# Optimization experiments

Hardware: AMD Instinct MI355X
Metric: run time of the kernel (lower is better)

## Reference

```python
import jax, jax.numpy as jnp
import numpy as np

D = 300       # word_embedding_dim
H = 15        # num_attention_heads
DK = D // H   # 20 per-head dim
QDIM = 200    # query_vector_dim (additive attention)
N_ITEMS = 100000
B, S = 1024, 50


def setup_inputs() -> dict:
    key = jax.random.key(0)
    ks = jax.random.split(key, 16)
    sc = 1.0 / np.sqrt(D)
    inp = {
        "user_news_id": jax.random.randint(ks[0], (B, S), 0, N_ITEMS, dtype=jnp.int64 if jax.config.jax_enable_x64 else jnp.int32),
        "user_vector": jax.random.normal(ks[1], (B, S, D), dtype=jnp.float32),
        # news-id embedding table, padding_idx=0 -> zero row
        "emb_table": jax.random.normal(ks[2], (N_ITEMS + 1, D), dtype=jnp.float32).at[0].set(0.0) * 0.02,
        # content Q/K/V projections
        "Wq": jax.random.normal(ks[3], (D, D), dtype=jnp.float32) * sc,
        "bq": jnp.zeros((D,), jnp.float32),
        "Wk": jax.random.normal(ks[4], (D, D), dtype=jnp.float32) * sc,
        "bk": jnp.zeros((D,), jnp.float32),
        "Wv": jax.random.normal(ks[5], (D, D), dtype=jnp.float32) * sc,
        "bv": jnp.zeros((D,), jnp.float32),
        # disentangled (news-id) Q/K projections
        "Wqp": jax.random.normal(ks[6], (D, D), dtype=jnp.float32) * sc,
        "bqp": jnp.zeros((D,), jnp.float32),
        "Wkp": jax.random.normal(ks[7], (D, D), dtype=jnp.float32) * sc,
        "bkp": jnp.zeros((D,), jnp.float32),
        # additive attention pooling params
        "W_add": jax.random.normal(ks[8], (D, QDIM), dtype=jnp.float32) * sc,
        "b_add": jnp.zeros((QDIM,), jnp.float32),
        "q_add": jax.random.normal(ks[9], (QDIM,), dtype=jnp.float32) * (1.0 / np.sqrt(QDIM)),
    }
    return inp


def _heads(x):
    # [B,S,D] -> [B,H,S,DK]
    b, s, _ = x.shape
    return x.reshape(b, s, H, DK).transpose(0, 2, 1, 3)


def reference(user_news_id, user_vector, emb_table, Wq, bq, Wk, bk, Wv, bv,
              Wqp, bqp, Wkp, bkp, W_add, b_add, q_add):
    # embedding lookup for clicked-news ids
    user_emb = emb_table[user_news_id]                      # [B,S,D]

    # content projections from user_vector, position/id projections from user_emb
    Qc = _heads(user_vector @ Wq + bq)
    Kc = _heads(user_vector @ Wk + bk)
    Vc = _heads(user_vector @ Wv + bv)
    Qp = _heads(user_emb @ Wqp + bqp)
    Kp = _heads(user_emb @ Wkp + bkp)

    # disentangled scores: content->content + content->id + id->content
    scores = (jnp.einsum("bhqd,bhkd->bhqk", Qc, Kc)
              + jnp.einsum("bhqd,bhkd->bhqk", Qc, Kp)
              + jnp.einsum("bhqd,bhkd->bhqk", Qp, Kc))
    scores = scores * (1.0 / np.sqrt(3.0 * DK))
    attn = jax.nn.softmax(scores, axis=-1)                  # [B,H,S,S]
    ctx = jnp.einsum("bhqk,bhkd->bhqd", attn, Vc)           # [B,H,S,DK]
    ctx = ctx.transpose(0, 2, 1, 3).reshape(user_vector.shape)  # [B,S,D]

    # additive attention pooling over the sequence
    t = jnp.tanh(ctx @ W_add + b_add)                       # [B,S,QDIM]
    a = jax.nn.softmax(t @ q_add, axis=-1)                  # [B,S]
    return jnp.einsum("bs,bsd->bd", a, ctx)                 # [B,D]
```

## Files before the change

### kernel.cpp

```cpp
#include <hip/hip_runtime.h>
#include <hip/hip_bf16.h>

#define SS   50
#define DD   300
#define NH   15
#define HD   20
#define QDIM 200

#define WSEG  97280
#define WAOFF 486400
#define WTOT  552960

typedef __attribute__((ext_vector_type(8)))  short bf8t;
typedef __attribute__((ext_vector_type(4)))  float f4t;
typedef __attribute__((ext_vector_type(16))) float f16t;

__device__ __forceinline__ unsigned short f2bf(float x){
  unsigned u = __float_as_uint(x);
  return (unsigned short)((u + 0x7fffu + ((u >> 16) & 1u)) >> 16);
}
__device__ __forceinline__ unsigned packbf(float a, float b){
  return (unsigned)f2bf(a) | ((unsigned)f2bf(b) << 16);
}
__device__ __forceinline__ f16t zero16(){
  f16t v;
  #pragma unroll
  for (int i = 0; i < 16; ++i) v[i] = 0.f;
  return v;
}

__global__ __launch_bounds__(256) void conv_weights(
    const float* __restrict__ Wq, const float* __restrict__ Wk,
    const float* __restrict__ Wv, const float* __restrict__ Wqp,
    const float* __restrict__ Wkp, const float* __restrict__ Wa,
    short* __restrict__ ws)
{
  int idx = blockIdx.x*256 + threadIdx.x;
  if (idx >= WTOT) return;
  float v = 0.f;
  if (idx < WAOFF){
    int seg = idx / WSEG, r = idx - seg*WSEG;
    int n = r / 320, k = r - n*320;
    const float* W = (seg==0)?Wq:(seg==1)?Wk:(seg==2)?Wv:(seg==3)?Wqp:Wkp;
    if (n < DD && k < DD) v = W[k*DD + n];
  } else {
    int r = idx - WAOFF;
    int n = r / 320, k = r - n*320;
    if (n < QDIM && k < DD) v = Wa[k*QDIM + n];
  }
  ws[idx] = (short)f2bf(v);
}

template<int NT, int NCTM>
__device__ __forceinline__ void gemm10(const unsigned char* sm, unsigned abase,
                                       const short* __restrict__ wt,
                                       int lane, int w, f4t (&acc)[NT][4])
{
  const int lm = lane & 15, lg = lane >> 4;
  #pragma unroll
  for (int step = 0; step < 10; ++step){
    bf8t a[4];
    #pragma unroll
    for (int rt = 0; rt < 4; ++rt)
      a[rt] = *(const bf8t*)(sm + abase + (unsigned)(rt*16 + lm)*656u + (unsigned)(step*32 + lg*8)*2u);
    #pragma unroll
    for (int t = 0; t < NT; ++t){
      int ct = w + t*8; if (ct > NCTM) ct = NCTM;
      bf8t bb = *(const bf8t*)(wt + (size_t)(ct*16 + lm)*320 + step*32 + lg*8);
      #pragma unroll
      for (int rt = 0; rt < 4; ++rt)
        acc[t][rt] = __builtin_amdgcn_mfma_f32_16x16x32_bf16(a[rt], bb, acc[t][rt], 0, 0, 0);
    }
  }
}

#define K1_UV  0
#define K1_UE  32800
#define K1_IDS 74784
#define K1_SM  74992

__global__ __launch_bounds__(512) void k1_proj(
    const int*   __restrict__ ids, const float* __restrict__ uv,
    const float* __restrict__ emb,
    const float* __restrict__ bq, const float* __restrict__ bk,
    const float* __restrict__ bv, const float* __restrict__ bqp,
    const float* __restrict__ bkp,
    const short* __restrict__ wsb,
    short* __restrict__ qg, short* __restrict__ kg, short* __restrict__ vg)
{
  __shared__ __align__(16) unsigned char sm[K1_SM];
  const int tid  = threadIdx.x;
  const int b    = blockIdx.x;
  const int w    = tid >> 6;
  const int lane = tid & 63;
  const int lm   = lane & 15, lg = lane >> 4;

  const short* wqT  = wsb;
  const short* wkT  = wsb + WSEG;
  const short* wvT  = wsb + 2*WSEG;
  const short* wqpT = wsb + 3*WSEG;
  const short* wkpT = wsb + 4*WSEG;

  if (tid < SS) *(int*)(sm + K1_IDS + tid*4) = ids[(size_t)b*SS + tid];
  {
    const float* srcv = uv + (size_t)b*SS*DD;
    for (int i = tid; i < SS*75; i += 512){
      int s = i/75, j4 = i - s*75;
      float4 v = *(const float4*)(srcv + s*DD + j4*4);
      *(unsigned*)(sm + K1_UV + (unsigned)s*656 + (unsigned)j4*8)     = packbf(v.x, v.y);
      *(unsigned*)(sm + K1_UV + (unsigned)s*656 + (unsigned)j4*8 + 4) = packbf(v.z, v.w);
    }
    for (int i = tid; i < SS*28; i += 512){
      int s = i/28, j = i - s*28;
      unsigned off = (j < 14) ? (K1_UV + (unsigned)s*656 + 600u + (unsigned)j*4)
                              : (K1_UE + (unsigned)s*656 + 600u + (unsigned)(j-14)*4);
      *(unsigned*)(sm + off) = 0;
    }
  }
  __syncthreads();
  for (int i = tid; i < SS*75; i += 512){
    int s = i/75, j4 = i - s*75;
    int id = *(const int*)(sm + K1_IDS + s*4);
    float4 v = *(const float4*)(emb + (size_t)id*DD + j4*4);
    *(unsigned*)(sm + K1_UE + (unsigned)s*656 + (unsigned)j4*8)     = packbf(v.x, v.y);
    *(unsigned*)(sm + K1_UE + (unsigned)s*656 + (unsigned)j4*8 + 4) = packbf(v.z, v.w);
  }
  __syncthreads();

  for (int i = tid; i < SS*15*4; i += 512){
    int row = i / 60, r2 = i - row*60;
    int head = r2 >> 2, j = r2 & 3;
    size_t base = ((size_t)b*SS + row)*720 + head*48 + 40 + j*2;
    *(unsigned*)(qg + base) = 0u;
    *(unsigned*)(kg + base) = 0u;
  }

  for (int u = w; u < 152; u += 8){
    const int g   = u / 38;
    const int rem = u - g*38;
    const int c   = rem >> 1, rh = rem & 1;
    const int col  = c*16 + lm;
    const int colc = (col < DD) ? col : DD-1;
    const bool valid = (col < DD);
    const int head = colc / HD;
    const int dd   = colc - head*HD;
    const unsigned abase = (g == 1) ? (unsigned)K1_UE : (unsigned)K1_UV;
    const short* wt = (g==0) ? wqT : (g==1) ? wqpT : (g==2) ? wvT : wkT;
    const short* wb = wt + (size_t)col*320 + lg*8;
    f4t a0 = {0.f,0.f,0.f,0.f}, a1 = {0.f,0.f,0.f,0.f};
    #pragma unroll
    for (int st = 0; st < 10; ++st){
      bf8t bb = *(const bf8t*)(wb + st*32);
      bf8t x0 = *(const bf8t*)(sm + abase + (unsigned)(rh*32 + lm)*656u + (unsigned)(st*32 + lg*8)*2u);
      bf8t x1 = *(const bf8t*)(sm + abase + (unsigned)(rh*32 + 16 + lm)*656u + (unsigned)(st*32 + lg*8)*2u);
      a0 = __builtin_amdgcn_mfma_f32_16x16x32_bf16(x0, bb, a0, 0, 0, 0);
      a1 = __builtin_amdgcn_mfma_f32_16x16x32_bf16(x1, bb, a1, 0, 0, 0);
    }
    if (g == 2){
      if (valid){
        float bias = bv[colc];
        #pragma unroll
        for (int i = 0; i < 4; ++i){
          int r0 = rh*32 + lg*4 + i;
          if (r0 < SS) vg[((size_t)b*SS + r0)*300 + col] = (short)f2bf(a0[i]+bias);
          int r1 = rh*32 + 16 + lg*4 + i;
          if (r1 < SS) vg[((size_t)b*SS + r1)*300 + col] = (short)f2bf(a1[i]+bias);
        }
      }
    } else if (g != 3){
      if (valid){
        float bias = (g==0) ? bq[colc] : bqp[colc];
        size_t qoff = (size_t)head*48 + dd + (g==1 ? 20 : 0);
        #pragma unroll
        for (int i = 0; i < 4; ++i){
          int r0 = rh*32 + lg*4 + i;
          if (r0 < SS) qg[((size_t)b*SS + r0)*720 + qoff] = (short)f2bf(a0[i]+bias);
          int r1 = rh*32 + 16 + lg*4 + i;
          if (r1 < SS) qg[((size_t)b*SS + r1)*720 + qoff] = (short)f2bf(a1[i]+bias);
        }
      }
    } else {
      float bkc = bk[colc];
      if (valid){
        size_t koff = (size_t)head*48 + 20 + dd;
        #pragma unroll
        for (int i = 0; i < 4; ++i){
          int r0 = rh*32 + lg*4 + i;
          if (r0 < SS) kg[((size_t)b*SS + r0)*720 + koff] = (short)f2bf(a0[i]+bkc);
          int r1 = rh*32 + 16 + lg*4 + i;
          if (r1 < SS) kg[((size_t)b*SS + r1)*720 + koff] = (short)f2bf(a1[i]+bkc);
        }
      }
      const short* wb2 = wkpT + (size_t)col*320 + lg*8;
      #pragma unroll
      for (int st = 0; st < 10; ++st){
        bf8t bb = *(const bf8t*)(wb2 + st*32);
        bf8t x0 = *(const bf8t*)(sm + K1_UE + (unsigned)(rh*32 + lm)*656u + (unsigned)(st*32 + lg*8)*2u);
        bf8t x1 = *(const bf8t*)(sm + K1_UE + (unsigned)(rh*32 + 16 + lm)*656u + (unsigned)(st*32 + lg*8)*2u);
        a0 = __builtin_amdgcn_mfma_f32_16x16x32_bf16(x0, bb, a0, 0, 0, 0);
        a1 = __builtin_amdgcn_mfma_f32_16x16x32_bf16(x1, bb, a1, 0, 0, 0);
      }
      if (valid){
        float bsum = bkc + bkp[colc];
        size_t koff = (size_t)head*48 + dd;
        #pragma unroll
        for (int i = 0; i < 4; ++i){
          int r0 = rh*32 + lg*4 + i;
          if (r0 < SS) kg[((size_t)b*SS + r0)*720 + koff] = (short)f2bf(a0[i]+bsum);
          int r1 = rh*32 + 16 + lg*4 + i;
          if (r1 < SS) kg[((size_t)b*SS + r1)*720 + koff] = (short)f2bf(a1[i]+bsum);
        }
      }
    }
  }
}

#define A_Q   0
#define A_K   20000
#define A_VT  40000
#define A_PBLK 4608
#define A_SM  53248

__global__ __launch_bounds__(512) void k2_attn(
    const short* __restrict__ qg, const short* __restrict__ kg,
    const short* __restrict__ vg, short* __restrict__ cg)
{
  __shared__ __align__(16) unsigned char sm[A_SM];
  const int tid  = threadIdx.x;
  const int bid  = blockIdx.x;
  const int b    = bid >> 2;
  const int hg   = bid & 3;
  const int nheads = (hg < 3) ? 4 : 3;
  const int w    = tid >> 6;
  const int lane = tid & 63;
  const int l31  = lane & 31, hi = lane >> 5;

  for (int i = tid; i < 828; i += 512)
    *(float4*)(sm + A_VT + (unsigned)i*16) = make_float4(0.f,0.f,0.f,0.f);
  __syncthreads();
  for (int i = tid; i < 2400; i += 512){
    int arr = (i < 1200) ? 0 : 1;
    int j = i - arr*1200;
    int row = j/24, c = j - row*24;
    const short* src = (arr ? kg : qg) + ((size_t)b*SS + row)*720 + hg*192 + c*8;
    float4 v = *(const float4*)src;
    *(float4*)(sm + (arr ? A_K : A_Q) + (unsigned)row*400 + (unsigned)c*16) = v;
  }
  for (int i = tid; i < 2000; i += 512){
    int row = i/40, d2 = i - row*40;
    unsigned v = *(const unsigned*)(vg + ((size_t)b*SS + row)*300 + hg*80 + d2*2);
    *(unsigned short*)(sm + A_VT + (unsigned)(d2*2)*144   + (unsigned)row*2) = (unsigned short)(v & 0xffffu);
    *(unsigned short*)(sm + A_VT + (unsigned)(d2*2+1)*144 + (unsigned)row*2) = (unsigned short)(v >> 16);
  }
  __syncthreads();

  const float rscale = 0.1290994449f;
  const int ahl = w >> 1, rt = w & 1;
  const bool act = (ahl < nheads);
  f16t s0, s1;
  if (act){
    s0 = zero16(); s1 = zero16();
    unsigned aoff = A_Q + (unsigned)(rt*32 + l31)*400 + (unsigned)ahl*96 + (unsigned)hi*16;
    unsigned koff = A_K + (unsigned)l31*400 + (unsigned)ahl*96 + (unsigned)hi*16;
    #pragma unroll
    for (int ks = 0; ks < 3; ++ks){
      bf8t a  = *(const bf8t*)(sm + aoff + ks*32);
      bf8t b0 = *(const bf8t*)(sm + koff + ks*32);
      bf8t b1 = *(const bf8t*)(sm + koff + 32u*400 + ks*32);
      s0 = __builtin_amdgcn_mfma_f32_32x32x16_bf16(a, b0, s0, 0, 0, 0);
      s1 = __builtin_amdgcn_mfma_f32_32x32x16_bf16(a, b1, s1, 0, 0, 0);
    }
  }
  __syncthreads();
  if (act){
    const bool m1 = (l31 >= 18);
    unsigned pb = (unsigned)w*A_PBLK;
    float rinv[16];
    #pragma unroll
    for (int r = 0; r < 16; ++r){
      int lrow = (r&3) + 8*(r>>2) + 4*hi;
      float v0 = s0[r]*rscale;
      float v1 = m1 ? -INFINITY : s1[r]*rscale;
      float mx = fmaxf(v0, v1);
      #pragma unroll
      for (int off = 1; off <= 16; off <<= 1) mx = fmaxf(mx, __shfl_xor(mx, off));
      float e0 = __expf(v0 - mx);
      float e1 = m1 ? 0.f : __expf(v1 - mx);
      float sum = e0 + e1;
      #pragma unroll
      for (int off = 1; off <= 16; off <<= 1) sum += __shfl_xor(sum, off);
      rinv[r] = 1.0f/sum;
      *(unsigned short*)(sm + pb + (unsigned)lrow*144 + (unsigned)l31*2)      = f2bf(e0);
      *(unsigned short*)(sm + pb + (unsigned)lrow*144 + 64 + (unsigned)l31*2) = f2bf(e1);
    }
    f16t c = zero16();
    unsigned pa  = pb + (unsigned)l31*144 + (unsigned)hi*16;
    unsigned vb2 = A_VT + (unsigned)(ahl*HD + l31)*144 + (unsigned)hi*16;
    #pragma unroll
    for (int ks = 0; ks < 4; ++ks){
      bf8t a = *(const bf8t*)(sm + pa + ks*32);
      bf8t v = *(const bf8t*)(sm + vb2 + ks*32);
      c = __builtin_amdgcn_mfma_f32_32x32x16_bf16(a, v, c, 0, 0, 0);
    }
    if (l31 < HD){
      int h = hg*4 + ahl;
      #pragma unroll
      for (int r = 0; r < 16; ++r){
        int q = rt*32 + (r&3) + 8*(r>>2) + 4*hi;
        if (q < SS)
          cg[((size_t)b*SS + q)*300 + h*HD + l31] = (short)f2bf(c[r]*rinv[r]);
      }
    }
  }
}

#define B_CTX 0
#define B_LG  41984
#define B_A2  44032
#define B_SM  44288

__global__ __launch_bounds__(512) void k3_pool(
    const short* __restrict__ cg, const short* __restrict__ wsb,
    const float* __restrict__ ba, const float* __restrict__ qa,
    float* __restrict__ out)
{
  __shared__ __align__(16) unsigned char sm[B_SM];
  const int tid  = threadIdx.x;
  const int b    = blockIdx.x;
  const int w    = tid >> 6;
  const int lane = tid & 63;
  const int lm   = lane & 15, lg = lane >> 4;
  const short* waT = wsb + WAOFF;

  for (int i = tid; i < SS*75; i += 512){
    int row = i/75, c = i - row*75;
    uint2 v = *(const uint2*)(cg + ((size_t)b*SS + row)*300 + c*4);
    *(uint2*)(sm + B_CTX + (unsigned)row*656 + (unsigned)c*8) = v;
  }
  for (int i = tid; i < SS*14; i += 512)
    *(unsigned*)(sm + B_CTX + (unsigned)(i/14)*656 + 600u + (unsigned)(i%14)*4) = 0;
  __syncthreads();

  {
    f4t accp[2][4];
    #pragma unroll
    for (int t = 0; t < 2; ++t)
      #pragma unroll
      for (int r = 0; r < 4; ++r) accp[t][r] = (f4t){0.f,0.f,0.f,0.f};
    gemm10<2,12>(sm, B_CTX, waT, lane, w, accp);
    float part[4][4];
    #pragma unroll
    for (int rt2 = 0; rt2 < 4; ++rt2)
      #pragma unroll
      for (int i = 0; i < 4; ++i) part[rt2][i] = 0.f;
    #pragma unroll
    for (int t = 0; t < 2; ++t){
      int ct = w + t*8; if (ct > 12) ct = 12;
      bool valid = (t == 0) || (w < 5);
      int col = ct*16 + lm;
      float bav = (col < QDIM) ? ba[col] : 0.f;
      float qav = (valid && col < QDIM) ? qa[col] : 0.f;
      #pragma unroll
      for (int rt2 = 0; rt2 < 4; ++rt2)
        #pragma unroll
        for (int i = 0; i < 4; ++i)
          part[rt2][i] += tanhf(accp[t][rt2][i] + bav) * qav;
    }
    #pragma unroll
    for (int off = 1; off <= 8; off <<= 1)
      #pragma unroll
      for (int rt2 = 0; rt2 < 4; ++rt2)
        #pragma unroll
        for (int i = 0; i < 4; ++i)
          part[rt2][i] += __shfl_xor(part[rt2][i], off);
    if (lm == 0){
      #pragma unroll
      for (int rt2 = 0; rt2 < 4; ++rt2)
        #pragma unroll
        for (int i = 0; i < 4; ++i){
          int row = rt2*16 + lg*4 + i;
          if (row < SS) *(float*)(sm + B_LG + (unsigned)(row*8 + w)*4) = part[rt2][i];
        }
    }
  }
  __syncthreads();
  if (w == 0){
    const int sl = lane < SS ? lane : SS - 1;
    const bool rowok = lane < SS;
    float lgv = -INFINITY;
    if (rowok){
      float s = 0.f;
      #pragma unroll
      for (int j = 0; j < 8; ++j) s += *(const float*)(sm + B_LG + (unsigned)(sl*8 + j)*4);
      lgv = s;
    }
    float m = lgv;
    #pragma unroll
    for (int off = 32; off; off >>= 1) m = fmaxf(m, __shfl_xor(m, off));
    float e = rowok ? __expf(lgv - m) : 0.f;
    float ssum = e;
    #pragma unroll
    for (int off = 32; off; off >>= 1) ssum += __shfl_xor(ssum, off);
    *(float*)(sm + B_A2 + lane*4) = e / ssum;
  }
  __syncthreads();
  if (tid < DD){
    float accv = 0.f;
    for (int s = 0; s < SS; ++s){
      float av = *(const float*)(sm + B_A2 + (unsigned)s*4);
      unsigned short cv = *(const unsigned short*)(sm + B_CTX + (unsigned)s*656 + (unsigned)tid*2);
      accv = fmaf(av, __uint_as_float((unsigned)cv << 16), accv);
    }
    out[(size_t)b*DD + tid] = accv;
  }
}

#define OFF_UV  0
#define OFF_UE  32800
#define QKSTR   400
#define OFF_Q   65600
#define OFF_K   85600
#define OFF_P   65600
#define PBLK    4608
#define PSTR    144
#define VTSTR   144
#define OFF_VT  105600
#define OFF_CTX 117120
#define OFF_LG  159104
#define OFF_A2  161152
#define OFF_IDS 161408
#define SM_TOTAL 161616

__global__ __launch_bounds__(512) void user_enc_kernel(
    const int*   __restrict__ ids, const float* __restrict__ uv,
    const float* __restrict__ emb,
    const float* __restrict__ bq, const float* __restrict__ bk,
    const float* __restrict__ bv, const float* __restrict__ bqp,
    const float* __restrict__ bkp,
    const float* __restrict__ ba, const float* __restrict__ qa,
    const short* __restrict__ wsb, float* __restrict__ out)
{
  __shared__ __align__(16) unsigned char sm[SM_TOTAL];
  const int tid  = threadIdx.x;
  const int b    = blockIdx.x;
  const int w    = tid >> 6;
  const int lane = tid & 63;
  const int lm   = lane & 15, lg = lane >> 4;
  const int l31  = lane & 31, hi = lane >> 5;

  const short* wqT  = wsb;
  const short* wkT  = wsb + WSEG;
  const short* wvT  = wsb + 2*WSEG;
  const short* wqpT = wsb + 3*WSEG;
  const short* wkpT = wsb + 4*WSEG;
  const short* waT  = wsb + WAOFF;

  if (tid < SS) *(int*)(sm + OFF_IDS + tid*4) = ids[(size_t)b*SS + tid];
  {
    const float* srcv = uv + (size_t)b*SS*DD;
    for (int i = tid; i < SS*75; i += 512){
      int s = i/75, j4 = i - s*75;
      float4 v = *(const float4*)(srcv + s*DD + j4*4);
      *(unsigned*)(sm + OFF_UV + (unsigned)s*656 + (unsigned)j4*8)     = packbf(v.x, v.y);
      *(unsigned*)(sm + OFF_UV + (unsigned)s*656 + (unsigned)j4*8 + 4) = packbf(v.z, v.w);
    }
    for (int i = tid; i < SS*28; i += 512){
      int s = i/28, j = i - s*28;
      unsigned off = (j < 14) ? (OFF_UV + (unsigned)s*656 + 600u + (unsigned)j*4)
                              : (OFF_UE + (unsigned)s*656 + 600u + (unsigned)(j-14)*4);
      *(unsigned*)(sm + off) = 0;
    }
    for (int i = tid; i < SS*14; i += 512)
      *(unsigned*)(sm + OFF_CTX + (unsigned)(i/14)*656 + 600u + (unsigned)(i%14)*4) = 0;
    for (int i = tid; i < 720; i += 512)
      *(float4*)(sm + OFF_VT + (unsigned)i*16) = make_float4(0.f,0.f,0.f,0.f);
  }
  __syncthreads();
  for (int i = tid; i < SS*75; i += 512){
    int s = i/75, j4 = i - s*75;
    int id = *(const int*)(sm + OFF_IDS + s*4);
    float4 v = *(const float4*)(emb + (size_t)id*DD + j4*4);
    *(unsigned*)(sm + OFF_UE + (unsigned)s*656 + (unsigned)j4*8)     = packbf(v.x, v.y);
    *(unsigned*)(sm + OFF_UE + (unsigned)s*656 + (unsigned)j4*8 + 4) = packbf(v.z, v.w);
  }

  const float rscale = 0.1290994449f;
  #pragma unroll 1
  for (int nb4 = 0; nb4 < 4; ++nb4){
    const int nheads = (nb4 < 3) ? 4 : 3;
    const int NCT    = (nb4 < 3) ? 5 : 4;
    __syncthreads();
    for (int i = tid; i < SS*4; i += 512){
      int r = i >> 2, hl0 = i & 3;
      *(float4*)(sm + OFF_Q + (unsigned)r*QKSTR + (unsigned)hl0*96 + 80) = make_float4(0.f,0.f,0.f,0.f);
      *(float4*)(sm + OFF_K + (unsigned)r*QKSTR + (unsigned)hl0*96 + 80) = make_float4(0.f,0.f,0.f,0.f);
    }
    for (int ht = w; ht < 8*NCT; ht += 8){
      const int g   = (ht >= 6*NCT) ? 3 : (ht >= 4*NCT) ? 2 : (ht >= 2*NCT) ? 1 : 0;
      const int rem = ht - g*2*NCT;
      const int c   = rem >> 1, rh = rem & 1;
      const int col = nb4*80 + c*16 + lm;
      const int colc = (col < DD) ? col : DD-1;
      const int head = col / HD;
      const int dd   = col - head*HD;
      const int hl   = head - nb4*4;
      const bool valid = (hl < nheads) && (col < DD);
      const unsigned abase = (g == 1) ? (unsigned)OFF_UE : (unsigned)OFF_UV;
      const short* wt = (g==0) ? wqT : (g==1) ? wqpT : (g==2) ? wvT : wkT;
      const short* wb = wt + (size_t)col*320 + lg*8;
      f4t a0 = {0.f,0.f,0.f,0.f}, a1 = {0.f,0.f,0.f,0.f};
      #pragma unroll
      for (int st = 0; st < 10; ++st){
        bf8t bb = *(const bf8t*)(wb + st*32);
        bf8t x0 = *(const bf8t*)(sm + abase + (unsigned)(rh*32 + lm)*656u + (unsigned)(st*32 + lg*8)*2u);
        bf8t x1 = *(const bf8t*)(sm + abase + (unsigned)(rh*32 + 16 + lm)*656u + (unsigned)(st*32 + lg*8)*2u);
        a0 = __builtin_amdgcn_mfma_f32_16x16x32_bf16(x0, bb, a0, 0, 0, 0);
        a1 = __builtin_amdgcn_mfma_f32_16x16x32_bf16(x1, bb, a1, 0, 0, 0);
      }
      if (g == 2){
        if (valid){
          float bias = bv[colc];
          unsigned vb = OFF_VT + (unsigned)(hl*HD + dd)*VTSTR;
          int r0 = rh*32 + lg*4;
          if (r0 < SS){
            *(unsigned*)(sm + vb + (unsigned)r0*2) = packbf(a0[0]+bias, a0[1]+bias);
            if (r0+2 < SS) *(unsigned*)(sm + vb + (unsigned)r0*2 + 4) = packbf(a0[2]+bias, a0[3]+bias);
          }
          int r1 = rh*32 + 16 + lg*4;
          if (r1 < SS){
            *(unsigned*)(sm + vb + (unsigned)r1*2) = packbf(a1[0]+bias, a1[1]+bias);
            if (r1+2 < SS) *(unsigned*)(sm + vb + (unsigned)r1*2 + 4) = packbf(a1[2]+bias, a1[3]+bias);
          }
        }
      } else if (g != 3){
        if (valid){
          float bias = (g==0) ? bq[colc] : bqp[colc];
          unsigned qb = OFF_Q + (unsigned)hl*96 + (unsigned)dd*2 + (g==1 ? 40u : 0u);
          #pragma unroll
          for (int i = 0; i < 4; ++i){
            int r0 = rh*32 + lg*4 + i;
            if (r0 < SS) *(unsigned short*)(sm + qb + (unsigned)r0*QKSTR) = f2bf(a0[i]+bias);
            int r1 = rh*32 + 16 + lg*4 + i;
            if (r1 < SS) *(unsigned short*)(sm + qb + (unsigned)r1*QKSTR) = f2bf(a1[i]+bias);
          }
        }
      } else {
        float bkc = bk[colc];
        if (valid){
          unsigned kb = OFF_K + (unsigned)hl*96 + (unsigned)dd*2 + 40u;
          #pragma unroll
          for (int i = 0; i < 4; ++i){
            int r0 = rh*32 + lg*4 + i;
            if (r0 < SS) *(unsigned short*)(sm + kb + (unsigned)r0*QKSTR) = f2bf(a0[i]+bkc);
            int r1 = rh*32 + 16 + lg*4 + i;
            if (r1 < SS) *(unsigned short*)(sm + kb + (unsigned)r1*QKSTR) = f2bf(a1[i]+bkc);
          }
        }
        const short* wb2 = wkpT + (size_t)col*320 + lg*8;
        #pragma unroll
        for (int st = 0; st < 10; ++st){
          bf8t bb = *(const bf8t*)(wb2 + st*32);
          bf8t x0 = *(const bf8t*)(sm + OFF_UE + (unsigned)(rh*32 + lm)*656u + (unsigned)(st*32 + lg*8)*2u);
          bf8t x1 = *(const bf8t*)(sm + OFF_UE + (unsigned)(rh*32 + 16 + lm)*656u + (unsigned)(st*32 + lg*8)*2u);
          a0 = __builtin_amdgcn_mfma_f32_16x16x32_bf16(x0, bb, a0, 0, 0, 0);
          a1 = __builtin_amdgcn_mfma_f32_16x16x32_bf16(x1, bb, a1, 0, 0, 0);
        }
        if (valid){
          float bsum = bkc + bkp[colc];
          unsigned kb = OFF_K + (unsigned)hl*96 + (unsigned)dd*2;
          #pragma unroll
          for (int i = 0; i < 4; ++i){
            int r0 = rh*32 + lg*4 + i;
            if (r0 < SS) *(unsigned short*)(sm + kb + (unsigned)r0*QKSTR) = f2bf(a0[i]+bsum);
            int r1 = rh*32 + 16 + lg*4 + i;
            if (r1 < SS) *(unsigned short*)(sm + kb + (unsigned)r1*QKSTR) = f2bf(a1[i]+bsum);
          }
        }
      }
    }
    __syncthreads();
    const int ahl = w >> 1, rt = w & 1;
    const bool act = (ahl < nheads);
    f16t s0, s1;
    if (act){
      s0 = zero16(); s1 = zero16();
      unsigned aoff = OFF_Q + (unsigned)(rt*32 + l31)*QKSTR + (unsigned)ahl*96 + (unsigned)hi*16;
      unsigned koff = OFF_K + (unsigned)l31*QKSTR + (unsigned)ahl*96 + (unsigned)hi*16;
      #pragma unroll
      for (int ks = 0; ks < 3; ++ks){
        bf8t a  = *(const bf8t*)(sm + aoff + ks*32);
        bf8t b0 = *(const bf8t*)(sm + koff + ks*32);
        bf8t b1 = *(const bf8t*)(sm + koff + 32u*QKSTR + ks*32);
        s0 = __builtin_amdgcn_mfma_f32_32x32x16_bf16(a, b0, s0, 0, 0, 0);
        s1 = __builtin_amdgcn_mfma_f32_32x32x16_bf16(a, b1, s1, 0, 0, 0);
      }
    }
    __syncthreads();
    if (act){
      const bool m1 = (l31 >= 18);
      unsigned pb = OFF_P + (unsigned)w*PBLK;
      float rinv[16];
      #pragma unroll
      for (int r = 0; r < 16; ++r){
        int lrow = (r&3) + 8*(r>>2) + 4*hi;
        float v0 = s0[r]*rscale;
        float v1 = m1 ? -INFINITY : s1[r]*rscale;
        float mx = fmaxf(v0, v1);
        #pragma unroll
        for (int off = 1; off <= 16; off <<= 1) mx = fmaxf(mx, __shfl_xor(mx, off));
        float e0 = __expf(v0 - mx);
        float e1 = m1 ? 0.f : __expf(v1 - mx);
        float sum = e0 + e1;
        #pragma unroll
        for (int off = 1; off <= 16; off <<= 1) sum += __shfl_xor(sum, off);
        rinv[r] = 1.0f/sum;
        *(unsigned short*)(sm + pb + (unsigned)lrow*PSTR + (unsigned)l31*2)      = f2bf(e0);
        *(unsigned short*)(sm + pb + (unsigned)lrow*PSTR + 64 + (unsigned)l31*2) = f2bf(e1);
      }
      f16t c = zero16();
      unsigned pa  = pb + (unsigned)l31*PSTR + (unsigned)hi*16;
      unsigned vb2 = OFF_VT + (unsigned)(ahl*HD + l31)*VTSTR + (unsigned)hi*16;
      #pragma unroll
      for (int ks = 0; ks < 4; ++ks){
        bf8t a = *(const bf8t*)(sm + pa + ks*32);
        bf8t v = *(const bf8t*)(sm + vb2 + ks*32);
        c = __builtin_amdgcn_mfma_f32_32x32x16_bf16(a, v, c, 0, 0, 0);
      }
      if (l31 < HD){
        int h = nb4*4 + ahl;
        #pragma unroll
        for (int r = 0; r < 16; ++r){
          int q = rt*32 + (r&3) + 8*(r>>2) + 4*hi;
          if (q < SS)
            *(unsigned short*)(sm + OFF_CTX + (unsigned)q*656 + (unsigned)(h*HD + l31)*2) =
                f2bf(c[r]*rinv[r]);
        }
      }
    }
  }
  __syncthreads();

  {
    f4t accp[2][4];
    #pragma unroll
    for (int t = 0; t < 2; ++t)
      #pragma unroll
      for (int r = 0; r < 4; ++r) accp[t][r] = (f4t){0.f,0.f,0.f,0.f};
    gemm10<2,12>(sm, OFF_CTX, waT, lane, w, accp);
    float part[4][4];
    #pragma unroll
    for (int rt2 = 0; rt2 < 4; ++rt2)
      #pragma unroll
      for (int i = 0; i < 4; ++i) part[rt2][i] = 0.f;
    #pragma unroll
    for (int t = 0; t < 2; ++t){
      int ct = w + t*8; if (ct > 12) ct = 12;
      bool valid = (t == 0) || (w < 5);
      int col = ct*16 + lm;
      float bav = (col < QDIM) ? ba[col] : 0.f;
      float qav = (valid && col < QDIM) ? qa[col] : 0.f;
      #pragma unroll
      for (int rt2 = 0; rt2 < 4; ++rt2)
        #pragma unroll
        for (int i = 0; i < 4; ++i)
          part[rt2][i] += tanhf(accp[t][rt2][i] + bav) * qav;
    }
    #pragma unroll
    for (int off = 1; off <= 8; off <<= 1)
      #pragma unroll
      for (int rt2 = 0; rt2 < 4; ++rt2)
        #pragma unroll
        for (int i = 0; i < 4; ++i)
          part[rt2][i] += __shfl_xor(part[rt2][i], off);
    if (lm == 0){
      #pragma unroll
      for (int rt2 = 0; rt2 < 4; ++rt2)
        #pragma unroll
        for (int i = 0; i < 4; ++i){
          int row = rt2*16 + lg*4 + i;
          if (row < SS) *(float*)(sm + OFF_LG + (unsigned)(row*8 + w)*4) = part[rt2][i];
        }
    }
  }
  __syncthreads();
  if (w == 0){
    const int sl = lane < SS ? lane : SS - 1;
    const bool rowok = lane < SS;
    float lgv = -INFINITY;
    if (rowok){
      float s = 0.f;
      #pragma unroll
      for (int j = 0; j < 8; ++j) s += *(const float*)(sm + OFF_LG + (unsigned)(sl*8 + j)*4);
      lgv = s;
    }
    float m = lgv;
    #pragma unroll
    for (int off = 32; off; off >>= 1) m = fmaxf(m, __shfl_xor(m, off));
    float e = rowok ? __expf(lgv - m) : 0.f;
    float ssum = e;
    #pragma unroll
    for (int off = 32; off; off >>= 1) ssum += __shfl_xor(ssum, off);
    *(float*)(sm + OFF_A2 + lane*4) = e / ssum;
  }
  __syncthreads();
  if (tid < DD){
    float accv = 0.f;
    for (int s = 0; s < SS; ++s){
      float av = *(const float*)(sm + OFF_A2 + (unsigned)s*4);
      unsigned short cv = *(const unsigned short*)(sm + OFF_CTX + (unsigned)s*656 + (unsigned)tid*2);
      accv = fmaf(av, __uint_as_float((unsigned)cv << 16), accv);
    }
    out[(size_t)b*DD + tid] = accv;
  }
}

extern "C" void kernel_launch(void* const* d_in, const int* in_sizes, int n_in,
                              void* d_out, int out_size, void* d_ws, size_t ws_size,
                              hipStream_t stream){
  (void)n_in; (void)out_size;
  const int*   ids = (const int*)  d_in[0];
  const float* uvp = (const float*)d_in[1];
  const float* emb = (const float*)d_in[2];
  const float* Wq  = (const float*)d_in[3];
  const float* bq  = (const float*)d_in[4];
  const float* Wk  = (const float*)d_in[5];
  const float* bk  = (const float*)d_in[6];
  const float* Wv  = (const float*)d_in[7];
  const float* bv  = (const float*)d_in[8];
  const float* Wqp = (const float*)d_in[9];
  const float* bqp = (const float*)d_in[10];
  const float* Wkp = (const float*)d_in[11];
  const float* bkp = (const float*)d_in[12];
  const float* Wa  = (const float*)d_in[13];
  const float* ba  = (const float*)d_in[14];
  const float* qa  = (const float*)d_in[15];
  short* wsb = (short*)d_ws;

  const int nb = in_sizes[0] / SS;
  const size_t wbytes = (size_t)WTOT * 2;
  const size_t qelems = (size_t)nb * SS * 720;
  const size_t velems = (size_t)nb * SS * 300;
  const size_t need   = wbytes + 2*qelems*2 + 2*velems*2;

  conv_weights<<<(WTOT + 255)/256, 256, 0, stream>>>(Wq, Wk, Wv, Wqp, Wkp, Wa, wsb);

  if (ws_size >= need){
    short* qg = (short*)((char*)d_ws + wbytes);
    short* kg = qg + qelems;
    short* vg = kg + qelems;
    short* cg = vg + velems;
    k1_proj<<<nb, 512, 0, stream>>>(ids, uvp, emb, bq, bk, bv, bqp, bkp,
                                    (const short*)wsb, qg, kg, vg);
    k2_attn<<<nb*4, 512, 0, stream>>>((const short*)qg, (const short*)kg,
                                      (const short*)vg, cg);
    k3_pool<<<nb, 512, 0, stream>>>((const short*)cg, (const short*)wsb,
                                    ba, qa, (float*)d_out);
  } else {
    user_enc_kernel<<<nb, 512, 0, stream>>>(ids, uvp, emb,
                                            bq, bk, bv, bqp, bkp, ba, qa,
                                            (const short*)wsb, (float*)d_out);
  }
}
```

Measured before the change: 397.9 us.

## Split projection kernel into five blocks per batch, one per projection

The projection kernel now launches five blocks per batch row, one per weight matrix (Q, Qp, V, K, Kp). Each block stages only the input it needs (user_vector or the gathered embedding), which cuts shared memory per block and allows higher occupancy. Kc and Kp are no longer summed inside k1; they are written to separate slots and the attention kernel combines them while loading K. The cost is that user_vector and the id-gathered embedding rows are each re-read by several blocks, and K loading in k2 does more arithmetic.

```diff
diff --git a/kernel.cpp b/kernel.cpp
--- a/kernel.cpp
+++ b/kernel.cpp
@@ -15,6 +15,8 @@
 typedef __attribute__((ext_vector_type(4)))  float f4t;
 typedef __attribute__((ext_vector_type(16))) float f16t;
 
+__device__ __forceinline__ float bflo(unsigned p){ return __uint_as_float(p << 16); }
+__device__ __forceinline__ float bfhi(unsigned p){ return __uint_as_float(p & 0xffff0000u); }
 __device__ __forceinline__ unsigned short f2bf(float x){
   unsigned u = __float_as_uint(x);
   return (unsigned short)((u + 0x7fffu + ((u >> 16) & 1u)) >> 16);
@@ -74,12 +76,10 @@
   }
 }
 
-#define K1_UV  0
-#define K1_UE  32800
-#define K1_IDS 74784
-#define K1_SM  74992
-
-__global__ __launch_bounds__(512) void k1_proj(
+#define P_IDS 32800
+#define P_SM  33008
+
+__global__ __launch_bounds__(512, 8) void k1_proj(
     const int*   __restrict__ ids, const float* __restrict__ uv,
     const float* __restrict__ emb,
     const float* __restrict__ bq, const float* __restrict__ bk,
@@ -88,128 +88,91 @@
     const short* __restrict__ wsb,
     short* __restrict__ qg, short* __restrict__ kg, short* __restrict__ vg)
 {
-  __shared__ __align__(16) unsigned char sm[K1_SM];
+  __shared__ __align__(16) unsigned char sm[P_SM];
   const int tid  = threadIdx.x;
-  const int b    = blockIdx.x;
+  const int bid  = blockIdx.x;
+  const int b    = bid / 5;
+  const int g    = bid - b*5;
   const int w    = tid >> 6;
   const int lane = tid & 63;
   const int lm   = lane & 15, lg = lane >> 4;
 
-  const short* wqT  = wsb;
-  const short* wkT  = wsb + WSEG;
-  const short* wvT  = wsb + 2*WSEG;
-  const short* wqpT = wsb + 3*WSEG;
-  const short* wkpT = wsb + 4*WSEG;
-
-  if (tid < SS) *(int*)(sm + K1_IDS + tid*4) = ids[(size_t)b*SS + tid];
-  {
+  if (tid < SS) *(int*)(sm + P_IDS + tid*4) = ids[(size_t)b*SS + tid];
+  __syncthreads();
+  const bool useUE = (g == 1) || (g == 4);
+  if (useUE){
+    for (int i = tid; i < SS*75; i += 512){
+      int s = i/75, j4 = i - s*75;
+      int id = *(const int*)(sm + P_IDS + s*4);
+      float4 v = *(const float4*)(emb + (size_t)id*DD + j4*4);
+      *(unsigned*)(sm + (unsigned)s*656 + (unsigned)j4*8)     = packbf(v.x, v.y);
+      *(unsigned*)(sm + (unsigned)s*656 + (unsigned)j4*8 + 4) = packbf(v.z, v.w);
+    }
+  } else {
     const float* srcv = uv + (size_t)b*SS*DD;
     for (int i = tid; i < SS*75; i += 512){
       int s = i/75, j4 = i - s*75;
       float4 v = *(const float4*)(srcv + s*DD + j4*4);
-      *(unsigned*)(sm + K1_UV + (unsigned)s*656 + (unsigned)j4*8)     = packbf(v.x, v.y);
-      *(unsigned*)(sm + K1_UV + (unsigned)s*656 + (unsigned)j4*8 + 4) = packbf(v.z, v.w);
-    }
-    for (int i = tid; i < SS*28; i += 512){
-      int s = i/28, j = i - s*28;
-      unsigned off = (j < 14) ? (K1_UV + (unsigned)s*656 + 600u + (unsigned)j*4)
-                              : (K1_UE + (unsigned)s*656 + 600u + (unsigned)(j-14)*4);
-      *(unsigned*)(sm + off) = 0;
-    }
-  }
-  __syncthreads();
-  for (int i = tid; i < SS*75; i += 512){
-    int s = i/75, j4 = i - s*75;
-    int id = *(const int*)(sm + K1_IDS + s*4);
-    float4 v = *(const float4*)(emb + (size_t)id*DD + j4*4);
-    *(unsigned*)(sm + K1_UE + (unsigned)s*656 + (unsigned)j4*8)     = packbf(v.x, v.y);
-    *(unsigned*)(sm + K1_UE + (unsigned)s*656 + (unsigned)j4*8 + 4) = packbf(v.z, v.w);
-  }
-  __syncthreads();
-
-  for (int i = tid; i < SS*15*4; i += 512){
-    int row = i / 60, r2 = i - row*60;
-    int head = r2 >> 2, j = r2 & 3;
-    size_t base = ((size_t)b*SS + row)*720 + head*48 + 40 + j*2;
-    *(unsigned*)(qg + base) = 0u;
-    *(unsigned*)(kg + base) = 0u;
-  }
-
-  for (int u = w; u < 152; u += 8){
-    const int g   = u / 38;
-    const int rem = u - g*38;
-    const int c   = rem >> 1, rh = rem & 1;
-    const int col  = c*16 + lm;
-    const int colc = (col < DD) ? col : DD-1;
+      *(unsigned*)(sm + (unsigned)s*656 + (unsigned)j4*8)     = packbf(v.x, v.y);
+      *(unsigned*)(sm + (unsigned)s*656 + (unsigned)j4*8 + 4) = packbf(v.z, v.w);
+    }
+  }
+  for (int i = tid; i < SS*14; i += 512)
+    *(unsigned*)(sm + (unsigned)(i/14)*656 + 600u + (unsigned)(i%14)*4) = 0;
+  if (g == 0 || g == 3){
+    short* pg = (g == 0) ? qg : kg;
+    for (int i = tid; i < 3000; i += 512){
+      int row = i/60, r = i - row*60;
+      int head = r >> 2, j = r & 3;
+      *(unsigned*)(pg + ((size_t)b*SS + row)*720 + head*48 + 40 + j*2) = 0u;
+    }
+  }
+  __syncthreads();
+
+  const int gseg = (g==0)?0:(g==1)?3:(g==2)?2:(g==3)?1:4;
+  const short* wt   = wsb + (size_t)gseg*WSEG;
+  const float* bias = (g==0)?bq:(g==1)?bqp:(g==2)?bv:(g==3)?bk:bkp;
+  short* dst = (g==2) ? vg : ((g < 2) ? qg : kg);
+  const int rowstride = (g==2) ? 300 : 720;
+  const int slot = (g==1 || g==3) ? 20 : 0;
+  short* drow0 = dst + (size_t)b*SS*rowstride;
+
+  for (int u = w; u < 38; u += 8){
+    const int c  = u >> 1, rh = u & 1;
+    const int col = c*16 + lm;
     const bool valid = (col < DD);
-    const int head = colc / HD;
-    const int dd   = colc - head*HD;
-    const unsigned abase = (g == 1) ? (unsigned)K1_UE : (unsigned)K1_UV;
-    const short* wt = (g==0) ? wqT : (g==1) ? wqpT : (g==2) ? wvT : wkT;
+    const int colc = valid ? col : DD-1;
     const short* wb = wt + (size_t)col*320 + lg*8;
+    int r0i = rh*32 + lm;       if (r0i > SS-1) r0i = SS-1;
+    int r1i = rh*32 + 16 + lm;  if (r1i > SS-1) r1i = SS-1;
+    const unsigned arow0 = (unsigned)r0i * 656u;
+    const unsigned arow1 = (unsigned)r1i * 656u;
     f4t a0 = {0.f,0.f,0.f,0.f}, a1 = {0.f,0.f,0.f,0.f};
     #pragma unroll
-    for (int st = 0; st < 10; ++st){
-      bf8t bb = *(const bf8t*)(wb + st*32);
-      bf8t x0 = *(const bf8t*)(sm + abase + (unsigned)(rh*32 + lm)*656u + (unsigned)(st*32 + lg*8)*2u);
-      bf8t x1 = *(const bf8t*)(sm + abase + (unsigned)(rh*32 + 16 + lm)*656u + (unsigned)(st*32 + lg*8)*2u);
-      a0 = __builtin_amdgcn_mfma_f32_16x16x32_bf16(x0, bb, a0, 0, 0, 0);
-      a1 = __builtin_amdgcn_mfma_f32_16x16x32_bf16(x1, bb, a1, 0, 0, 0);
-    }
-    if (g == 2){
-      if (valid){
-        float bias = bv[colc];
-        #pragma unroll
-        for (int i = 0; i < 4; ++i){
-          int r0 = rh*32 + lg*4 + i;
-          if (r0 < SS) vg[((size_t)b*SS + r0)*300 + col] = (short)f2bf(a0[i]+bias);
-          int r1 = rh*32 + 16 + lg*4 + i;
-          if (r1 < SS) vg[((size_t)b*SS + r1)*300 + col] = (short)f2bf(a1[i]+bias);
-        }
-      }
-    } else if (g != 3){
-      if (valid){
-        float bias = (g==0) ? bq[colc] : bqp[colc];
-        size_t qoff = (size_t)head*48 + dd + (g==1 ? 20 : 0);
-        #pragma unroll
-        for (int i = 0; i < 4; ++i){
-          int r0 = rh*32 + lg*4 + i;
-          if (r0 < SS) qg[((size_t)b*SS + r0)*720 + qoff] = (short)f2bf(a0[i]+bias);
-          int r1 = rh*32 + 16 + lg*4 + i;
-          if (r1 < SS) qg[((size_t)b*SS + r1)*720 + qoff] = (short)f2bf(a1[i]+bias);
-        }
-      }
-    } else {
-      float bkc = bk[colc];
-      if (valid){
-        size_t koff = (size_t)head*48 + 20 + dd;
-        #pragma unroll
-        for (int i = 0; i < 4; ++i){
-          int r0 = rh*32 + lg*4 + i;
-          if (r0 < SS) kg[((size_t)b*SS + r0)*720 + koff] = (short)f2bf(a0[i]+bkc);
-          int r1 = rh*32 + 16 + lg*4 + i;
-          if (r1 < SS) kg[((size_t)b*SS + r1)*720 + koff] = (short)f2bf(a1[i]+bkc);
-        }
-      }
-      const short* wb2 = wkpT + (size_t)col*320 + lg*8;
-      #pragma unroll
-      for (int st = 0; st < 10; ++st){
-        bf8t bb = *(const bf8t*)(wb2 + st*32);
-        bf8t x0 = *(const bf8t*)(sm + K1_UE + (unsigned)(rh*32 + lm)*656u + (unsigned)(st*32 + lg*8)*2u);
-        bf8t x1 = *(const bf8t*)(sm + K1_UE + (unsigned)(rh*32 + 16 + lm)*656u + (unsigned)(st*32 + lg*8)*2u);
-        a0 = __builtin_amdgcn_mfma_f32_16x16x32_bf16(x0, bb, a0, 0, 0, 0);
-        a1 = __builtin_amdgcn_mfma_f32_16x16x32_bf16(x1, bb, a1, 0, 0, 0);
-      }
-      if (valid){
-        float bsum = bkc + bkp[colc];
-        size_t koff = (size_t)head*48 + dd;
-        #pragma unroll
-        for (int i = 0; i < 4; ++i){
-          int r0 = rh*32 + lg*4 + i;
-          if (r0 < SS) kg[((size_t)b*SS + r0)*720 + koff] = (short)f2bf(a0[i]+bsum);
-          int r1 = rh*32 + 16 + lg*4 + i;
-          if (r1 < SS) kg[((size_t)b*SS + r1)*720 + koff] = (short)f2bf(a1[i]+bsum);
-        }
+    for (int h2 = 0; h2 < 2; ++h2){
+      bf8t wr[5];
+      #pragma unroll
+      for (int st = 0; st < 5; ++st) wr[st] = *(const bf8t*)(wb + (h2*5 + st)*32);
+      #pragma unroll
+      for (int st = 0; st < 5; ++st){
+        unsigned coff = (unsigned)((h2*5 + st)*32 + lg*8)*2u;
+        bf8t x0 = *(const bf8t*)(sm + arow0 + coff);
+        bf8t x1 = *(const bf8t*)(sm + arow1 + coff);
+        a0 = __builtin_amdgcn_mfma_f32_16x16x32_bf16(x0, wr[st], a0, 0, 0, 0);
+        a1 = __builtin_amdgcn_mfma_f32_16x16x32_bf16(x1, wr[st], a1, 0, 0, 0);
+      }
+    }
+    if (valid){
+      float bb = bias[colc];
+      int head = colc / HD, dd = colc - head*HD;
+      size_t coff = (g==2) ? (size_t)col : (size_t)head*48 + dd + slot;
+      short* dcol = drow0 + coff;
+      #pragma unroll
+      for (int i = 0; i < 4; ++i){
+        int r0 = rh*32 + lg*4 + i;
+        if (r0 < SS) dcol[(size_t)r0*rowstride] = (short)f2bf(a0[i] + bb);
+        int r1 = rh*32 + 16 + lg*4 + i;
+        if (r1 < SS) dcol[(size_t)r1*rowstride] = (short)f2bf(a1[i] + bb);
       }
     }
   }
@@ -238,13 +201,25 @@
   for (int i = tid; i < 828; i += 512)
     *(float4*)(sm + A_VT + (unsigned)i*16) = make_float4(0.f,0.f,0.f,0.f);
   __syncthreads();
-  for (int i = tid; i < 2400; i += 512){
-    int arr = (i < 1200) ? 0 : 1;
-    int j = i - arr*1200;
-    int row = j/24, c = j - row*24;
-    const short* src = (arr ? kg : qg) + ((size_t)b*SS + row)*720 + hg*192 + c*8;
-    float4 v = *(const float4*)src;
-    *(float4*)(sm + (arr ? A_K : A_Q) + (unsigned)row*400 + (unsigned)c*16) = v;
+  for (int i = tid; i < 1200; i += 512){
+    int row = i/24, c = i - row*24;
+    const short* src = qg + ((size_t)b*SS + row)*720 + hg*192 + c*8;
+    *(float4*)(sm + A_Q + (unsigned)row*400 + (unsigned)c*16) = *(const float4*)src;
+  }
+  for (int i = tid; i < 4800; i += 512){
+    int rhd = i / 24, j = i - rhd*24;
+    int row = rhd >> 2, hl = rhd & 3;
+    const short* base = kg + ((size_t)b*SS + row)*720 + (hg*4 + hl)*48;
+    unsigned char* ldst = sm + A_K + (unsigned)row*400 + (unsigned)hl*96;
+    if (j < 10){
+      unsigned kp = *(const unsigned*)(base + j*2);
+      unsigned kc = *(const unsigned*)(base + 20 + j*2);
+      *(unsigned*)(ldst + j*4) = packbf(bflo(kp)+bflo(kc), bfhi(kp)+bfhi(kc));
+    } else if (j < 20){
+      *(unsigned*)(ldst + 40 + (j-10)*4) = *(const unsigned*)(base + 20 + (j-10)*2);
+    } else {
+      *(unsigned*)(ldst + 80 + (j-20)*4) = 0u;
+    }
   }
   for (int i = tid; i < 2000; i += 512){
     int row = i/40, d2 = i - row*40;
@@ -749,8 +724,8 @@
     short* kg = qg + qelems;
     short* vg = kg + qelems;
     short* cg = vg + velems;
-    k1_proj<<<nb, 512, 0, stream>>>(ids, uvp, emb, bq, bk, bv, bqp, bkp,
-                                    (const short*)wsb, qg, kg, vg);
+    k1_proj<<<nb*5, 512, 0, stream>>>(ids, uvp, emb, bq, bk, bv, bqp, bkp,
+                                      (const short*)wsb, qg, kg, vg);
     k2_attn<<<nb*4, 512, 0, stream>>>((const short*)qg, (const short*)kg,
                                       (const short*)vg, cg);
     k3_pool<<<nb, 512, 0, stream>>>((const short*)cg, (const short*)wsb,
```

After: 461.8 us (median of 2 runs). +16.1%, slower.
